# Kernel tuning notes

Hardware: AMD Instinct MI355X
Metric: run time of the kernel (lower is better)

The kernel has to match this reference:

```python
import jax, jax.numpy as jnp
import numpy as np

B, T, C, D = 16, 2048, 1024, 64

def setup_inputs() -> dict:
    key = jax.random.key(0)
    kx, kq, kk, kv = jax.random.split(key, 4)
    x = jax.random.normal(kx, (B, T, C), dtype=jnp.float32)
    # nn.Linear(emb_size, head_size, bias=False): y = x @ W, store W as [C, D]
    s = 1.0 / np.sqrt(C)
    Wq = jax.random.normal(kq, (C, D), dtype=jnp.float32) * s
    Wk = jax.random.normal(kk, (C, D), dtype=jnp.float32) * s
    Wv = jax.random.normal(kv, (C, D), dtype=jnp.float32) * s
    return {"x": x, "Wq": Wq, "Wk": Wk, "Wv": Wv}

def reference(x, Wq, Wk, Wv):
    Bv, Tv, Cv = x.shape
    q = jnp.einsum('btc,cd->btd', x, Wq)
    k = jnp.einsum('btc,cd->btd', x, Wk)
    v = jnp.einsum('btc,cd->btd', x, Wv)
    # NOTE: original scales by C**0.5 (emb_size), not head_size**0.5
    scores = jnp.einsum('bqd,bkd->bqk', q, k) / jnp.sqrt(jnp.float32(Cv))
    causal = jnp.tril(jnp.ones((Tv, Tv), dtype=bool))
    scores = jnp.where(causal[None, :, :], scores, -jnp.inf)
    weights = jax.nn.softmax(scores, axis=-1)
    # dropout(p=0.4) omitted: reference assumes eval mode (identity)
    return jnp.einsum('bqk,bkd->bqd', weights, v)
```

## Files before the change

kernel.cpp:

```cpp
#include <hip/hip_runtime.h>
#include <math.h>


#define B_ 16
#define T_ 2048
#define C_ 1024
#define D_ 64
#define BT_ (B_ * T_)

typedef __attribute__((ext_vector_type(8))) short short8;
typedef __attribute__((ext_vector_type(4))) float f32x4;

__device__ __forceinline__ unsigned short f2bf(float f) {
    unsigned u = __float_as_uint(f);
    return (unsigned short)((u + 0x7fffu + ((u >> 16) & 1u)) >> 16);
}
__device__ __forceinline__ float bf2f(unsigned short h) {
    return __uint_as_float(((unsigned)h) << 16);
}
#define MFMA16(a, b, c) __builtin_amdgcn_mfma_f32_16x16x32_bf16((a), (b), (c), 0, 0, 0)

__global__ __launch_bounds__(256) void wprep_kernel(
    const float* __restrict__ Wq, const float* __restrict__ Wk,
    const float* __restrict__ Wv, short* __restrict__ WTh, short* __restrict__ WTl)
{
    __shared__ float ws[64][65];
    const int bid = blockIdx.x, tid = threadIdx.x;
    const int wi = bid >> 4, ct = bid & 15, c0 = ct * 64;
    const float* W = (wi == 0) ? Wq : (wi == 1) ? Wk : Wv;
    #pragma unroll
    for (int i = 0; i < 4; ++i) {
        int rr = (tid >> 4) + i * 16;
        int dd = (tid & 15) * 4;
        *(float4*)&ws[rr][dd] = *(const float4*)&W[(size_t)(c0 + rr) * 64 + dd];
    }
    __syncthreads();
    const int d = tid >> 2, cc0 = (tid & 3) * 16;
    short8 h0, h1, l0, l1;
    #pragma unroll
    for (int i = 0; i < 8; ++i) {
        float v = ws[cc0 + i][d];
        unsigned short hh = f2bf(v);
        h0[i] = (short)hh; l0[i] = (short)f2bf(v - bf2f(hh));
        float v2 = ws[cc0 + 8 + i][d];
        unsigned short hh2 = f2bf(v2);
        h1[i] = (short)hh2; l1[i] = (short)f2bf(v2 - bf2f(hh2));
    }
    size_t o = (size_t)(wi * 64 + d) * 1024 + c0 + cc0;
    *(short8*)&WTh[o] = h0; *(short8*)&WTh[o + 8] = h1;
    *(short8*)&WTl[o] = l0; *(short8*)&WTl[o + 8] = l1;
}

__global__ __launch_bounds__(256) void qkv_mfma_kernel(
    const float* __restrict__ x, const short* __restrict__ WTh,
    const short* __restrict__ WTl, float* __restrict__ qf,
    short* __restrict__ kbf, short* __restrict__ vtb)
{
    __shared__ alignas(16) short xh[32 * 64];
    __shared__ alignas(16) short xl[32 * 64];

    const int tid = threadIdx.x;
    const int row0 = blockIdx.x * 32;
    const int lane = tid & 63, w = tid >> 6;
    const int lr = lane & 15, lg = lane >> 4;
    const int sr = tid >> 3, sc = (tid & 7) * 8;

    f32x4 acc[2][3];
    #pragma unroll
    for (int mt = 0; mt < 2; ++mt)
        #pragma unroll
        for (int gi = 0; gi < 3; ++gi) acc[mt][gi] = (f32x4){0.f, 0.f, 0.f, 0.f};

    for (int kb = 0; kb < C_; kb += 64) {
        float xv[8];
        const float* xp = &x[(size_t)(row0 + sr) * C_ + kb + sc];
        *(float4*)&xv[0] = *(const float4*)&xp[0];
        *(float4*)&xv[4] = *(const float4*)&xp[4];
        short8 h0, l0;
        #pragma unroll
        for (int i = 0; i < 8; ++i) {
            unsigned short hh = f2bf(xv[i]);
            h0[i] = (short)hh; l0[i] = (short)f2bf(xv[i] - bf2f(hh));
        }
        __syncthreads();
        {
            int u0 = (sc >> 3) ^ (sr & 7);
            *(short8*)&xh[sr * 64 + u0 * 8] = h0;
            *(short8*)&xl[sr * 64 + u0 * 8] = l0;
        }
        __syncthreads();

        #pragma unroll
        for (int kc = 0; kc < 2; ++kc) {
            short8 ah[2], al[2];
            #pragma unroll
            for (int mt = 0; mt < 2; ++mt) {
                int r = mt * 16 + lr;
                int usw = (kc * 4 + lg) ^ (r & 7);
                ah[mt] = *(short8*)&xh[r * 64 + usw * 8];
                al[mt] = *(short8*)&xl[r * 64 + usw * 8];
            }
            #pragma unroll
            for (int gi = 0; gi < 3; ++gi) {
                int n = (3 * w + gi) * 16 + lr;
                size_t wo = (size_t)n * 1024 + kb + kc * 32 + lg * 8;
                short8 wh = *(const short8*)&WTh[wo];
                short8 wl = *(const short8*)&WTl[wo];
                #pragma unroll
                for (int mt = 0; mt < 2; ++mt) {
                    acc[mt][gi] = MFMA16(ah[mt], wh, acc[mt][gi]);
                    acc[mt][gi] = MFMA16(ah[mt], wl, acc[mt][gi]);
                    acc[mt][gi] = MFMA16(al[mt], wh, acc[mt][gi]);
                }
            }
        }
    }

    #pragma unroll
    for (int mt = 0; mt < 2; ++mt) {
        int rbase = row0 + mt * 16 + lg * 4;
        #pragma unroll
        for (int gi = 0; gi < 3; ++gi) {
            int g = 3 * w + gi;
            f32x4 a = acc[mt][gi];
            int col = g * 16 + lr;
            if (g < 4) {
                #pragma unroll
                for (int reg = 0; reg < 4; ++reg)
                    qf[(size_t)(rbase + reg) * 64 + col] = a[reg];
            } else if (g < 8) {
                #pragma unroll
                for (int reg = 0; reg < 4; ++reg)
                    kbf[(size_t)(rbase + reg) * 64 + (col - 64)] = (short)f2bf(a[reg]);
            } else {
                int d = col - 128;
                int bb = rbase >> 11, t0 = rbase & (T_ - 1);
                short4 pk;
                pk.x = (short)f2bf(a[0]); pk.y = (short)f2bf(a[1]);
                pk.z = (short)f2bf(a[2]); pk.w = (short)f2bf(a[3]);
                *(short4*)&vtb[((size_t)(bb * 64 + d) << 11) + t0] = pk;
            }
        }
    }
}

__global__ __launch_bounds__(256) void attn_mfma_kernel(
    const float* __restrict__ qf, const short* __restrict__ kbf,
    const short* __restrict__ vtb, float* __restrict__ out)
{
    __shared__ alignas(16) short pbuf[4 * 16 * 64];

    const int bid = blockIdx.x;
    const int b  = bid & 15;
    const int pp = (bid >> 4) & 31;
    const int sw = (bid >> 8) & 1;
    const int tid = threadIdx.x;
    const int lane = tid & 63, w = tid >> 6;
    const int lr = lane & 15, lg = lane >> 4;

    const int sel = w >> 1;
    const int hv  = (w & 1) ^ sw;
    const int t   = hv ? (127 - 2 * pp - sel) : (2 * pp + sel);
    const int trow0 = t * 16;
    const int njt = (t >> 2) + 1;

    const size_t base_tok = (size_t)b * T_;
    const short* Kb = kbf + base_tok * 64;
    const short* Vb = vtb + (size_t)b * 64 * T_;
    short* pw = pbuf + w * 16 * 64;

    short8 qh[2], ql[2];
    #pragma unroll
    for (int kc = 0; kc < 2; ++kc) {
        const float* qp = &qf[(base_tok + trow0 + lr) * 64 + kc * 32 + lg * 8];
        float4 q0 = *(const float4*)qp;
        float4 q1 = *(const float4*)(qp + 4);
        float qs[8] = {q0.x, q0.y, q0.z, q0.w, q1.x, q1.y, q1.z, q1.w};
        #pragma unroll
        for (int i = 0; i < 8; ++i) {
            float v = qs[i] * 0.03125f;
            unsigned short hh = f2bf(v);
            qh[kc][i] = (short)hh;
            ql[kc][i] = (short)f2bf(v - bf2f(hh));
        }
    }

    f32x4 o[4];
    #pragma unroll
    for (int dt = 0; dt < 4; ++dt) o[dt] = (f32x4){0.f, 0.f, 0.f, 0.f};
    float m[4]    = {-INFINITY, -INFINITY, -INFINITY, -INFINITY};
    float lsum[4] = {0.f, 0.f, 0.f, 0.f};

    short8 kfA[2][4], kfB[2][4];
    auto loadK = [&](short8 (&kf)[2][4], int jt) {
        int j0 = jt * 64;
        #pragma unroll
        for (int kc = 0; kc < 2; ++kc)
            #pragma unroll
            for (int nt = 0; nt < 4; ++nt)
                kf[kc][nt] = *(const short8*)
                    &Kb[(size_t)(j0 + nt * 16 + lr) * 64 + kc * 32 + lg * 8];
    };

    auto doTile = [&](short8 (&kf)[2][4], short8 (&kfn)[2][4], int jt) {
        f32x4 sx[4];
        #pragma unroll
        for (int nt = 0; nt < 4; ++nt) sx[nt] = (f32x4){0.f, 0.f, 0.f, 0.f};
        #pragma unroll
        for (int kc = 0; kc < 2; ++kc)
            #pragma unroll
            for (int nt = 0; nt < 4; ++nt) {
                sx[nt] = MFMA16(qh[kc], kf[kc][nt], sx[nt]);
                sx[nt] = MFMA16(ql[kc], kf[kc][nt], sx[nt]);
            }

        const int j0 = jt * 64;
        short8 vf[4][2];
        #pragma unroll
        for (int dt = 0; dt < 4; ++dt)
            #pragma unroll
            for (int kc = 0; kc < 2; ++kc)
                vf[dt][kc] = *(const short8*)
                    &Vb[(size_t)(dt * 16 + lr) * T_ + j0 + kc * 32 + lg * 8];
        if (jt + 1 < njt) loadK(kfn, jt + 1);

        if (jt == njt - 1) {
            #pragma unroll
            for (int nt = 0; nt < 4; ++nt) {
                int j = j0 + nt * 16 + lr;
                #pragma unroll
                for (int reg = 0; reg < 4; ++reg)
                    if (j > trow0 + lg * 4 + reg) sx[nt][reg] = -INFINITY;
            }
        }

        float corr[4], psum[4] = {0.f, 0.f, 0.f, 0.f};
        #pragma unroll
        for (int reg = 0; reg < 4; ++reg) {
            float vmax = fmaxf(fmaxf(sx[0][reg], sx[1][reg]),
                               fmaxf(sx[2][reg], sx[3][reg]));
            vmax = fmaxf(vmax, __shfl_xor(vmax, 1));
            vmax = fmaxf(vmax, __shfl_xor(vmax, 2));
            vmax = fmaxf(vmax, __shfl_xor(vmax, 4));
            vmax = fmaxf(vmax, __shfl_xor(vmax, 8));
            float mnew = fmaxf(m[reg], vmax);
            corr[reg] = __expf(m[reg] - mnew);
            m[reg] = mnew;
        }
        #pragma unroll
        for (int nt = 0; nt < 4; ++nt)
            #pragma unroll
            for (int reg = 0; reg < 4; ++reg) {
                float p = __expf(sx[nt][reg] - m[reg]);
                psum[reg] += p;
                int qr = lg * 4 + reg;
                int colj = nt * 16 + lr;
                int usw = (colj >> 3) ^ (qr & 7);
                pw[qr * 64 + usw * 8 + (colj & 7)] = (short)f2bf(p);
            }
        #pragma unroll
        for (int reg = 0; reg < 4; ++reg)
            lsum[reg] = lsum[reg] * corr[reg] + psum[reg];
        #pragma unroll
        for (int dt = 0; dt < 4; ++dt) {
            o[dt][0] *= corr[0]; o[dt][1] *= corr[1];
            o[dt][2] *= corr[2]; o[dt][3] *= corr[3];
        }

        asm volatile("s_waitcnt lgkmcnt(0)" ::: "memory");
        __builtin_amdgcn_sched_barrier(0);
        short8 pf[2];
        #pragma unroll
        for (int kc = 0; kc < 2; ++kc) {
            int usw = (kc * 4 + lg) ^ (lr & 7);
            pf[kc] = *(short8*)&pw[lr * 64 + usw * 8];
        }
        #pragma unroll
        for (int dt = 0; dt < 4; ++dt)
            #pragma unroll
            for (int kc = 0; kc < 2; ++kc)
                o[dt] = MFMA16(pf[kc], vf[dt][kc], o[dt]);
    };

    loadK(kfA, 0);
    int jt = 0;
    while (true) {
        doTile(kfA, kfB, jt);
        if (++jt == njt) break;
        doTile(kfB, kfA, jt);
        if (++jt == njt) break;
    }

    #pragma unroll
    for (int reg = 0; reg < 4; ++reg) {
        lsum[reg] += __shfl_xor(lsum[reg], 1);
        lsum[reg] += __shfl_xor(lsum[reg], 2);
        lsum[reg] += __shfl_xor(lsum[reg], 4);
        lsum[reg] += __shfl_xor(lsum[reg], 8);
        lsum[reg] = 1.f / lsum[reg];
    }
    #pragma unroll
    for (int dt = 0; dt < 4; ++dt)
        #pragma unroll
        for (int reg = 0; reg < 4; ++reg)
            out[(base_tok + trow0 + lg * 4 + reg) * 64 + dt * 16 + lr] =
                o[dt][reg] * lsum[reg];
}

extern "C" void kernel_launch(void* const* d_in, const int* in_sizes, int n_in,
                              void* d_out, int out_size, void* d_ws, size_t ws_size,
                              hipStream_t stream) {
    const float* x  = (const float*)d_in[0];
    const float* Wq = (const float*)d_in[1];
    const float* Wk = (const float*)d_in[2];
    const float* Wv = (const float*)d_in[3];
    float* out = (float*)d_out;

    float* qf  = (float*)d_ws;
    short* kbf = (short*)(qf + (size_t)BT_ * 64);
    short* vtb = kbf + (size_t)BT_ * 64;
    short* WTh = vtb + (size_t)BT_ * 64;
    short* WTl = WTh + (size_t)192 * 1024;

    wprep_kernel<<<48, 256, 0, stream>>>(Wq, Wk, Wv, WTh, WTl);
    qkv_mfma_kernel<<<1024, 256, 0, stream>>>(x, WTh, WTl, qf, kbf, vtb);
    attn_mfma_kernel<<<512, 256, 0, stream>>>(qf, kbf, vtb, out);
}
```

Baseline: 326.8 us.

## Double-buffer x tiles and enlarge QKV projection row tile to 64

The QKV projection kernel now processes 64 rows per block instead of 32, halving the grid and doubling the reuse of each weight fragment loaded from global memory. It double-buffers the split-bf16 x tile in LDS and prefetches the next tile's global loads into registers, so one barrier per k-step replaces two. Weight fragments for the whole k-step are hoisted ahead of the MFMAs. This raises register and LDS use per block, which can lower occupancy, and 512 blocks gives fewer waves to hide latency.

New measurement: 297.4 us. -9.0%, faster.

```diff
diff --git a/kernel.cpp b/kernel.cpp
--- a/kernel.cpp
+++ b/kernel.cpp
@@ -56,68 +56,92 @@
     const short* __restrict__ WTl, float* __restrict__ qf,
     short* __restrict__ kbf, short* __restrict__ vtb)
 {
-    __shared__ alignas(16) short xh[32 * 64];
-    __shared__ alignas(16) short xl[32 * 64];
+    __shared__ alignas(16) short xh[2][64 * 64];
+    __shared__ alignas(16) short xl[2][64 * 64];
 
     const int tid = threadIdx.x;
-    const int row0 = blockIdx.x * 32;
+    const int row0 = blockIdx.x * 64;
     const int lane = tid & 63, w = tid >> 6;
     const int lr = lane & 15, lg = lane >> 4;
-    const int sr = tid >> 3, sc = (tid & 7) * 8;
-
-    f32x4 acc[2][3];
-    #pragma unroll
-    for (int mt = 0; mt < 2; ++mt)
+    const int sr = tid >> 2, sc = (tid & 3) * 16;
+
+    f32x4 acc[4][3];
+    #pragma unroll
+    for (int mt = 0; mt < 4; ++mt)
         #pragma unroll
         for (int gi = 0; gi < 3; ++gi) acc[mt][gi] = (f32x4){0.f, 0.f, 0.f, 0.f};
 
-    for (int kb = 0; kb < C_; kb += 64) {
-        float xv[8];
-        const float* xp = &x[(size_t)(row0 + sr) * C_ + kb + sc];
-        *(float4*)&xv[0] = *(const float4*)&xp[0];
-        *(float4*)&xv[4] = *(const float4*)&xp[4];
-        short8 h0, l0;
+    const float* xrow = &x[(size_t)(row0 + sr) * C_ + sc];
+
+    float xv[16];
+    auto issue_loads = [&](int kb) {
+        *(float4*)&xv[0]  = *(const float4*)&xrow[kb];
+        *(float4*)&xv[4]  = *(const float4*)&xrow[kb + 4];
+        *(float4*)&xv[8]  = *(const float4*)&xrow[kb + 8];
+        *(float4*)&xv[12] = *(const float4*)&xrow[kb + 12];
+    };
+    auto convert_write = [&](int buf) {
+        short8 h0, h1, l0, l1;
         #pragma unroll
         for (int i = 0; i < 8; ++i) {
             unsigned short hh = f2bf(xv[i]);
             h0[i] = (short)hh; l0[i] = (short)f2bf(xv[i] - bf2f(hh));
-        }
+            unsigned short hh2 = f2bf(xv[8 + i]);
+            h1[i] = (short)hh2; l1[i] = (short)f2bf(xv[8 + i] - bf2f(hh2));
+        }
+        int u0 = sc >> 3, u1 = u0 + 1;
+        *(short8*)&xh[buf][sr * 64 + ((u0 ^ (sr & 7)) * 8)] = h0;
+        *(short8*)&xh[buf][sr * 64 + ((u1 ^ (sr & 7)) * 8)] = h1;
+        *(short8*)&xl[buf][sr * 64 + ((u0 ^ (sr & 7)) * 8)] = l0;
+        *(short8*)&xl[buf][sr * 64 + ((u1 ^ (sr & 7)) * 8)] = l1;
+    };
+
+    issue_loads(0);
+    convert_write(0);
+    issue_loads(64);
+
+    for (int t = 0; t < 16; ++t) {
         __syncthreads();
-        {
-            int u0 = (sc >> 3) ^ (sr & 7);
-            *(short8*)&xh[sr * 64 + u0 * 8] = h0;
-            *(short8*)&xl[sr * 64 + u0 * 8] = l0;
-        }
-        __syncthreads();
-
-        #pragma unroll
-        for (int kc = 0; kc < 2; ++kc) {
-            short8 ah[2], al[2];
-            #pragma unroll
-            for (int mt = 0; mt < 2; ++mt) {
-                int r = mt * 16 + lr;
-                int usw = (kc * 4 + lg) ^ (r & 7);
-                ah[mt] = *(short8*)&xh[r * 64 + usw * 8];
-                al[mt] = *(short8*)&xl[r * 64 + usw * 8];
-            }
+        if (t < 15) convert_write((t + 1) & 1);
+        if (t < 14) issue_loads((t + 2) * 64);
+
+        const int kb = t * 64;
+        const int bsel = t & 1;
+
+        short8 wfh[2][3], wfl[2][3];
+        #pragma unroll
+        for (int kc = 0; kc < 2; ++kc)
             #pragma unroll
             for (int gi = 0; gi < 3; ++gi) {
                 int n = (3 * w + gi) * 16 + lr;
                 size_t wo = (size_t)n * 1024 + kb + kc * 32 + lg * 8;
-                short8 wh = *(const short8*)&WTh[wo];
-                short8 wl = *(const short8*)&WTl[wo];
+                wfh[kc][gi] = *(const short8*)&WTh[wo];
+                wfl[kc][gi] = *(const short8*)&WTl[wo];
+            }
+
+        #pragma unroll
+        for (int kc = 0; kc < 2; ++kc) {
+            short8 ah[4], al[4];
+            #pragma unroll
+            for (int mt = 0; mt < 4; ++mt) {
+                int r = mt * 16 + lr;
+                int usw = (kc * 4 + lg) ^ (r & 7);
+                ah[mt] = *(short8*)&xh[bsel][r * 64 + usw * 8];
+                al[mt] = *(short8*)&xl[bsel][r * 64 + usw * 8];
+            }
+            #pragma unroll
+            for (int gi = 0; gi < 3; ++gi)
                 #pragma unroll
-                for (int mt = 0; mt < 2; ++mt) {
-                    acc[mt][gi] = MFMA16(ah[mt], wh, acc[mt][gi]);
-                    acc[mt][gi] = MFMA16(ah[mt], wl, acc[mt][gi]);
-                    acc[mt][gi] = MFMA16(al[mt], wh, acc[mt][gi]);
+                for (int mt = 0; mt < 4; ++mt) {
+                    acc[mt][gi] = MFMA16(ah[mt], wfh[kc][gi], acc[mt][gi]);
+                    acc[mt][gi] = MFMA16(ah[mt], wfl[kc][gi], acc[mt][gi]);
+                    acc[mt][gi] = MFMA16(al[mt], wfh[kc][gi], acc[mt][gi]);
                 }
-            }
-        }
-    }
-
-    #pragma unroll
-    for (int mt = 0; mt < 2; ++mt) {
+        }
+    }
+
+    #pragma unroll
+    for (int mt = 0; mt < 4; ++mt) {
         int rbase = row0 + mt * 16 + lg * 4;
         #pragma unroll
         for (int gi = 0; gi < 3; ++gi) {
@@ -323,6 +347,6 @@
     short* WTl = WTh + (size_t)192 * 1024;
 
     wprep_kernel<<<48, 256, 0, stream>>>(Wq, Wk, Wv, WTh, WTl);
-    qkv_mfma_kernel<<<1024, 256, 0, stream>>>(x, WTh, WTl, qf, kbf, vtb);
+    qkv_mfma_kernel<<<512, 256, 0, stream>>>(x, WTh, WTl, qf, kbf, vtb);
     attn_mfma_kernel<<<512, 256, 0, stream>>>(qf, kbf, vtb, out);
 }
```
